# Optimization experiments

Hardware: AMD Instinct MI355X
Metric: run time of the kernel (lower is better)

## Reference

```python
import jax, jax.numpy as jnp
import numpy as np

SLOPE = 0.01

def leaky_tanh(x):
    return jnp.tanh(x * (2.0 / 3.0)) * 1.7159 + x * SLOPE

def lstm_cell(x, h, c, w_ih, w_hh, b_ih, b_hh):
    # torch LSTMCell gate order: i, f, g, o
    gates = x @ w_ih.T + b_ih + h @ w_hh.T + b_hh
    i, f, g, o = jnp.split(gates, 4, axis=-1)
    c_new = jax.nn.sigmoid(f) * c + jax.nn.sigmoid(i) * jnp.tanh(g)
    h_new = jax.nn.sigmoid(o) * jnp.tanh(c_new)
    return h_new, c_new

def setup_inputs() -> dict:
    key = jax.random.key(0)
    ks = jax.random.split(key, 16)
    T, B, I, H, O = 512, 64, 128, 2048, 64
    H1, H2 = H // 2, H // 8  # 1024, 256
    F2 = H // 4              # 512
    s = 0.02
    return {
        "inputs": jax.random.normal(ks[0], (T, B, I), dtype=jnp.float32),
        "fc1_w": jax.random.normal(ks[1], (H, I), dtype=jnp.float32) * s,
        "fc1_b": jax.random.normal(ks[2], (H,), dtype=jnp.float32) * s,
        "w_ih1": jax.random.normal(ks[3], (4 * H1, H), dtype=jnp.float32) * s,
        "w_hh1": jax.random.normal(ks[4], (4 * H1, H1), dtype=jnp.float32) * s,
        "b_ih1": jax.random.normal(ks[5], (4 * H1,), dtype=jnp.float32) * s,
        "b_hh1": jax.random.normal(ks[6], (4 * H1,), dtype=jnp.float32) * s,
        "fc2_w": jax.random.normal(ks[7], (F2, H1), dtype=jnp.float32) * s,
        "fc2_b": jax.random.normal(ks[8], (F2,), dtype=jnp.float32) * s,
        "w_ih2": jax.random.normal(ks[9], (4 * H2, F2), dtype=jnp.float32) * s,
        "w_hh2": jax.random.normal(ks[10], (4 * H2, H2), dtype=jnp.float32) * s,
        "b_ih2": jax.random.normal(ks[11], (4 * H2,), dtype=jnp.float32) * s,
        "b_hh2": jax.random.normal(ks[12], (4 * H2,), dtype=jnp.float32) * s,
        "fc3_w": jax.random.normal(ks[13], (O, H2), dtype=jnp.float32) * s,
        "fc3_b": jax.random.normal(ks[14], (O,), dtype=jnp.float32) * s,
    }

def reference(inputs, fc1_w, fc1_b, w_ih1, w_hh1, b_ih1, b_hh1,
              fc2_w, fc2_b, w_ih2, w_hh2, b_ih2, b_hh2, fc3_w, fc3_b):
    T, B, _ = inputs.shape
    H1 = w_hh1.shape[1]
    H2 = w_hh2.shape[1]
    h1 = jnp.zeros((B, H1), dtype=inputs.dtype)
    c1 = jnp.zeros((B, H1), dtype=inputs.dtype)
    h2 = jnp.zeros((B, H2), dtype=inputs.dtype)
    c2 = jnp.zeros((B, H2), dtype=inputs.dtype)

    def step(carry, xt):
        h1, c1, h2, c2 = carry
        x = leaky_tanh(xt @ fc1_w.T + fc1_b)
        h1, c1 = lstm_cell(x, h1, c1, w_ih1, w_hh1, b_ih1, b_hh1)
        x = leaky_tanh(h1 @ fc2_w.T + fc2_b)
        h2, c2 = lstm_cell(x, h2, c2, w_ih2, w_hh2, b_ih2, b_hh2)
        yhat = h2 @ fc3_w.T + fc3_b
        return (h1, c1, h2, c2), yhat

    _, outputs = jax.lax.scan(step, (h1, c1, h2, c2), inputs)
    return outputs  # [T, B, output_size]
```

## Files before the change

kernel.cpp:

```cpp
#include <hip/hip_runtime.h>
#include <hip/hip_bf16.h>

static constexpr int T_  = 512;
static constexpr int B_  = 64;
static constexpr int I_  = 128;
static constexpr int H_  = 2048;
static constexpr int H1_ = 1024;
static constexpr int F2_ = 512;
static constexpr int H2_ = 256;
static constexpr int O_  = 64;
static constexpr int G1N = 4096;
static constexpr int G2N = 1024;
static constexpr int NW  = 176;

typedef __attribute__((ext_vector_type(8))) __bf16 bfx8;
typedef __attribute__((ext_vector_type(4))) __bf16 bfx4;
typedef __attribute__((ext_vector_type(4))) float  fx4;

#define DEV __device__ __forceinline__

DEV fx4 mfma16(bfx8 a, bfx8 b, fx4 c) {
  return __builtin_amdgcn_mfma_f32_16x16x32_bf16(a, b, c, 0, 0, 0);
}
DEV float fast_sig(float x) { return 1.0f / (1.0f + __expf(-x)); }
DEV float fast_tanh(float x) {
  x = fminf(fmaxf(x, -30.0f), 30.0f);
  return 2.0f / (1.0f + __expf(-2.0f * x)) - 1.0f;
}
DEV float leaky_tanh_(float x) { return fast_tanh(x * (2.0f / 3.0f)) * 1.7159f + 0.01f * x; }

DEV void gld16(const void* g, void* l) {
  __builtin_amdgcn_global_load_lds(
      (const __attribute__((address_space(1))) unsigned int*)g,
      (__attribute__((address_space(3))) unsigned int*)l, 16, 0, 0);
}
DEV void gld16c(const void* g, void* l) {
  __builtin_amdgcn_global_load_lds(
      (const __attribute__((address_space(1))) unsigned int*)g,
      (__attribute__((address_space(3))) unsigned int*)l, 16, 0, 17);
}
DEV void spin_ge(int* p, int tgt) {
  while (__hip_atomic_load(p, __ATOMIC_RELAXED, __HIP_MEMORY_SCOPE_AGENT) < tgt)
    __builtin_amdgcn_s_sleep(1);
}
DEV void stc2(unsigned short* p, unsigned short v) {
  __hip_atomic_store(p, v, __ATOMIC_RELAXED, __HIP_MEMORY_SCOPE_AGENT);
}
DEV unsigned long long ldc8(const void* p) {
  return __hip_atomic_load((const unsigned long long*)p, __ATOMIC_RELAXED,
                           __HIP_MEMORY_SCOPE_AGENT);
}
DEV unsigned short bf16bits(float f) {
  __bf16 h = (__bf16)f;
  return __builtin_bit_cast(unsigned short, h);
}
DEV void arrive1(int* p) {
  __hip_atomic_fetch_add(p, 1, __ATOMIC_RELAXED, __HIP_MEMORY_SCOPE_AGENT);
}

__global__ void k_f2b(const float* __restrict__ s, __bf16* __restrict__ d, int n4) {
  int i = blockIdx.x * blockDim.x + threadIdx.x;
  int st = gridDim.x * blockDim.x;
  for (; i < n4; i += st) {
    float4 v = ((const float4*)s)[i];
    bfx4 o = { (__bf16)v.x, (__bf16)v.y, (__bf16)v.z, (__bf16)v.w };
    ((bfx4*)d)[i] = o;
  }
}
__global__ void k_add2(const float* __restrict__ a, const float* __restrict__ b,
                       float* __restrict__ d, int n) {
  int i = blockIdx.x * blockDim.x + threadIdx.x;
  if (i < n) d[i] = a[i] + b[i];
}

__global__ void k_wre1(const float* __restrict__ w, __bf16* __restrict__ W2) {
  int v = blockIdx.x * 256 + threadIdx.x;
  int l = v & 63, kk = (v >> 6) & 31, g = (v >> 11) & 3, ng = v >> 13;
  int row = g * 1024 + ng * 16 + (l & 15);
  int k0  = kk * 32 + (l >> 4) * 8;
  const float* sp = w + (size_t)row * 1024 + k0;
  float4 v0 = ((const float4*)sp)[0];
  float4 v1 = ((const float4*)sp)[1];
  bfx8 o = { (__bf16)v0.x, (__bf16)v0.y, (__bf16)v0.z, (__bf16)v0.w,
             (__bf16)v1.x, (__bf16)v1.y, (__bf16)v1.z, (__bf16)v1.w };
  *(bfx8*)(W2 + (size_t)v * 8) = o;
}

DEV void gemm_tile(char* sm, const __bf16* __restrict__ A, const __bf16* __restrict__ W,
                   __bf16* __restrict__ outB, const float* __restrict__ bias,
                   int m0, int n0, int N, int K, int epi, int wt)
{
  char* As = sm;
  char* Ws = sm + 16384;
  const int tid = threadIdx.x, lane = tid & 63, wave = tid >> 6;
  const int wm = wave >> 1, wn = wave & 1;
  const int rr = lane & 15, hi = lane >> 4;
  fx4 acc[4][4] = {};
  for (int k0 = 0; k0 < K; k0 += 64) {
    __syncthreads();
#pragma unroll
    for (int i = 0; i < 4; ++i) {
      int idx = i * 256 + tid;
      int r = idx >> 3, cs = (idx & 7) ^ (r & 7);
      gld16(A + (size_t)(m0 + r) * K + k0 + cs * 8, As + idx * 16);
      gld16(W + (size_t)(n0 + r) * K + k0 + cs * 8, Ws + idx * 16);
    }
    __syncthreads();
#pragma unroll
    for (int kh = 0; kh < 2; ++kh) {
      bfx8 a[4], b[4];
      const int cg = kh * 4 + hi;
#pragma unroll
      for (int mi = 0; mi < 4; ++mi) {
        int ra = wm * 64 + mi * 16 + rr;
        a[mi] = *(const bfx8*)(As + ra * 128 + ((cg ^ (ra & 7)) << 4));
      }
#pragma unroll
      for (int ni = 0; ni < 4; ++ni) {
        int rb = wn * 64 + ni * 16 + rr;
        b[ni] = *(const bfx8*)(Ws + rb * 128 + ((cg ^ (rb & 7)) << 4));
      }
#pragma unroll
      for (int mi = 0; mi < 4; ++mi)
#pragma unroll
        for (int ni = 0; ni < 4; ++ni)
          acc[mi][ni] = mfma16(a[mi], b[ni], acc[mi][ni]);
    }
  }
  const int cr = hi * 4, cc = rr;
#pragma unroll
  for (int mi = 0; mi < 4; ++mi)
#pragma unroll
    for (int ni = 0; ni < 4; ++ni) {
      int col = n0 + wn * 64 + ni * 16 + cc;
#pragma unroll
      for (int r = 0; r < 4; ++r) {
        int row = m0 + wm * 64 + mi * 16 + cr + r;
        float v = acc[mi][ni][r] + bias[col];
        if (epi == 1) v = leaky_tanh_(v);
        if (wt) stc2((unsigned short*)outB + ((size_t)row * N + col), bf16bits(v));
        else    outB[(size_t)row * N + col] = (__bf16)v;
      }
    }
}

__launch_bounds__(256)
__global__ void k_gemm(const __bf16* __restrict__ A, const __bf16* __restrict__ W,
                       __bf16* __restrict__ outB, const float* __restrict__ bias,
                       int M, int N, int K, int epi)
{
  __shared__ __align__(16) char sm[32768];
  (void)M;
  gemm_tile(sm, A, W, outB, bias, blockIdx.y * 128, blockIdx.x * 128, N, K, epi, 0);
}

DEV void stage(char* dst, int rsB, const __bf16* __restrict__ src, size_t sStride,
               int n, int lg) {
  for (int idx = threadIdx.x; idx < n; idx += 256) {
    int r = idx >> lg, c = idx & ((1 << lg) - 1);
    *(bfx8*)(dst + r * rsB + ((c * 16) ^ ((r & 7) << 4))) =
        *(const bfx8*)(src + (size_t)r * sStride + c * 8);
  }
}

struct KP {
  const __bf16 *W2, *whh2b;
  const __bf16 *g1rd;  __bf16 *g1wr;
  const __bf16 *xcrd;  __bf16 *xcwr;
  const __bf16 *infc1;
  const __bf16 *h1rd;  const __bf16 *h1s0;  __bf16 *h1wr;
  __bf16 *x2c; __bf16 *g2;
  const __bf16 *wfc1, *wih1, *wfc2, *wih2;
  const float *bfc1, *bs1, *bfc2, *bs2;
  float *c1, *c2;
  __bf16 *h2a;
  int *cnt;
  int Tc, t2base, do_l1, do_l2, do_fc2, do_ih1, do_fc1;
};

__launch_bounds__(256, 1)
__global__ void k_persist3(KP p)
{
  __shared__ __align__(16) char smem[131072];
  const int tid = threadIdx.x, lane = tid & 63, wv = tid >> 6;
  const int rr = lane & 15, hi = lane >> 4;
  const int col = tid & 15, brow = tid >> 4;
  const int bid = blockIdx.x;
  int* cnt = p.cnt;
  const int Tc = p.Tc;

  if (bid < 64) {
    if (!p.do_l1) return;
    const int ng = bid;
    char* As = smem;
    float* Cp = (float*)smem;

    bfx8 wreg[4][8];
#pragma unroll
    for (int g = 0; g < 4; ++g)
#pragma unroll
      for (int j = 0; j < 8; ++j)
        wreg[g][j] = *(const bfx8*)(p.W2 + (size_t)((ng * 4 + g) * 32 + wv * 8 + j) * 512 + lane * 8);

    float pc[4];
#pragma unroll
    for (int q = 0; q < 4; ++q)
      pc[q] = p.c1[(brow + q * 16) * 1024 + ng * 16 + col];

    for (int s = 0; s < Tc; ++s) {
      float pg[4][4];
#pragma unroll
      for (int q = 0; q < 4; ++q)
#pragma unroll
        for (int g = 0; g < 4; ++g)
          pg[q][g] = (float)p.g1rd[(size_t)(s * 64 + brow + q * 16) * 4096 + g * 1024 + ng * 16 + col];

      if (s > 0 && tid < 4) spin_ge(cnt + tid * 128, 16 * s);
      __syncthreads();

      const __bf16* h1s = (s == 0) ? p.h1s0 : (p.h1wr + (size_t)s * 65536);
      {
        char* dstb = smem + wv * 32768;
#pragma unroll 8
        for (int i = 0; i < 32; ++i) {
          int d = wv * 2048 + i * 64 + lane;
          int r = d >> 7;
          int sg = (r << 7) | ((d & 127) ^ (r & 7));
          gld16c(h1s + (size_t)sg * 8, dstb + i * 1024);
        }
      }
      __syncthreads();

      fx4 acc[4][4] = {};
#pragma unroll
      for (int j = 0; j < 8; ++j) {
        const int kB = (wv * 8 + j) * 64 + hi * 16;
        bfx8 a[4];
#pragma unroll
        for (int m = 0; m < 4; ++m) {
          int ra = m * 16 + rr;
          a[m] = *(const bfx8*)(As + ra * 2048 + (kB ^ ((ra & 7) << 4)));
        }
#pragma unroll
        for (int g = 0; g < 4; ++g)
#pragma unroll
          for (int m = 0; m < 4; ++m)
            acc[g][m] = mfma16(a[m], wreg[g][j], acc[g][m]);
      }
      __syncthreads();
#pragma unroll
      for (int g = 0; g < 4; ++g)
#pragma unroll
        for (int m = 0; m < 4; ++m) {
          int gc = g * 16 + rr;
          int bx = (m * 16 + hi * 4) ^ ((gc & 15) << 2);
          *(fx4*)(Cp + ((wv * 64 + gc) * 64 + bx)) = acc[g][m];
        }
      __syncthreads();

      __bf16* h1o = p.h1wr + (size_t)(s + 1) * 65536;
#pragma unroll
      for (int q = 0; q < 4; ++q) {
        int b_ = brow + q * 16;
        float gv[4];
#pragma unroll
        for (int g = 0; g < 4; ++g) {
          int gc = g * 16 + col;
          int bx = b_ ^ ((gc & 15) << 2);
          float v = pg[q][g];
#pragma unroll
          for (int w = 0; w < 4; ++w)
            v += Cp[(w * 64 + gc) * 64 + bx];
          gv[g] = v;
        }
        float cn = fast_sig(gv[1]) * pc[q] + fast_sig(gv[0]) * fast_tanh(gv[2]);
        pc[q] = cn;
        float hv = fast_sig(gv[3]) * fast_tanh(cn);
        stc2((unsigned short*)h1o + (b_ * 1024 + ng * 16 + col), bf16bits(hv));
      }
      __syncthreads();
      if (tid == 0) arrive1(cnt + (ng & 3) * 128);
    }
#pragma unroll
    for (int q = 0; q < 4; ++q)
      p.c1[(brow + q * 16) * 1024 + ng * 16 + col] = pc[q];

  } else if (bid < 80) {
    if (!p.do_l2) return;
    const int ng2 = bid - 64;
    char* Ws2 = smem;
    char* As2 = smem + 32768;
    float (*Gx2)[64][16] = (float (*)[64][16])(smem + 32768);

    for (int idx = tid; idx < 2048; idx += 256) {
      int r = idx >> 5, c = idx & 31;
      int wr = (r >> 4) * 256 + ng2 * 16 + (r & 15);
      *(bfx8*)(Ws2 + r * 512 + ((c * 16) ^ ((r & 7) << 4))) =
          *(const bfx8*)(p.whh2b + (size_t)wr * 256 + c * 8);
    }
    float pc2[4];
#pragma unroll
    for (int q = 0; q < 4; ++q)
      pc2[q] = p.c2[(brow + q * 16) * 256 + ng2 * 16 + col];

    if (tid == 0) spin_ge(cnt + 640, NW);
    __syncthreads();

    for (int s = 0; s < Tc; ++s) {
      float pg[4][4];
#pragma unroll
      for (int q = 0; q < 4; ++q)
#pragma unroll
        for (int g = 0; g < 4; ++g)
          pg[q][g] = (float)p.g2[(size_t)(s * 64 + brow + q * 16) * 1024 + g * 256 + ng2 * 16 + col];

      if (s > 0 && tid == 0) spin_ge(cnt + 512, 16 * s);
      __syncthreads();

      const __bf16* h2s = p.h2a + (size_t)(p.t2base + s) * 16384;
      for (int idx = tid; idx < 2048; idx += 256) {
        int r = idx >> 5, c = idx & 31;
        const char* sp = (const char*)(h2s + r * 256 + c * 8);
        unsigned long long lo = ldc8(sp), hi8 = ldc8(sp + 8);
        char* dp = As2 + r * 512 + ((c * 16) ^ ((r & 7) << 4));
        *(unsigned long long*)dp = lo;
        *(unsigned long long*)(dp + 8) = hi8;
      }
      __syncthreads();

      fx4 acc[4] = {};
#pragma unroll
      for (int ks = 0; ks < 8; ++ks) {
        const int cb = ks * 64 + hi * 16;
        int rb = wv * 16 + rr;
        bfx8 bfr = *(const bfx8*)(Ws2 + rb * 512 + (cb ^ ((rb & 7) << 4)));
#pragma unroll
        for (int m = 0; m < 4; ++m) {
          int ra = m * 16 + rr;
          bfx8 afr = *(const bfx8*)(As2 + ra * 512 + (cb ^ ((ra & 7) << 4)));
          acc[m] = mfma16(afr, bfr, acc[m]);
        }
      }
      __syncthreads();
#pragma unroll
      for (int m = 0; m < 4; ++m)
#pragma unroll
        for (int r = 0; r < 4; ++r)
          Gx2[wv][m * 16 + hi * 4 + r][rr] = acc[m][r];
      __syncthreads();

      __bf16* h2o = p.h2a + (size_t)(p.t2base + s + 1) * 16384;
#pragma unroll
      for (int q = 0; q < 4; ++q) {
        int b_ = brow + q * 16;
        float gi = Gx2[0][b_][col] + pg[q][0];
        float gf = Gx2[1][b_][col] + pg[q][1];
        float gg = Gx2[2][b_][col] + pg[q][2];
        float go = Gx2[3][b_][col] + pg[q][3];
        float cn = fast_sig(gf) * pc2[q] + fast_sig(gi) * fast_tanh(gg);
        pc2[q] = cn;
        float hv = fast_sig(go) * fast_tanh(cn);
        stc2((unsigned short*)h2o + (b_ * 256 + ng2 * 16 + col), bf16bits(hv));
      }
      __syncthreads();
      if (tid == 0) arrive1(cnt + 512);
    }
#pragma unroll
    for (int q = 0; q < 4; ++q)
      p.c2[(brow + q * 16) * 256 + ng2 * 16 + col] = pc2[q];

  } else {
    const int wid = bid - 80;
    const int Mt = (Tc * 64) / 128;
    if (p.do_fc2) {
      for (int i = wid; i < Mt * 4; i += NW)
        gemm_tile(smem, p.h1rd + 65536, p.wfc2, p.x2c, p.bfc2,
                  (i >> 2) * 128, (i & 3) * 128, F2_, H1_, 1, 1);
      __syncthreads();
      if (tid == 0) { arrive1(cnt + 576); spin_ge(cnt + 576, NW); }
      __syncthreads();
      for (int i = wid; i < Mt * 8; i += NW)
        gemm_tile(smem, p.x2c, p.wih2, p.g2, p.bs2,
                  (i >> 3) * 128, (i & 7) * 128, G2N, F2_, 0, 1);
      __syncthreads();
      if (tid == 0) arrive1(cnt + 640);
    }
    if (p.do_ih1) {
      for (int i = wid; i < Mt * 32; i += NW)
        gemm_tile(smem, p.xcrd, p.wih1, p.g1wr, p.bs1,
                  (i >> 5) * 128, (i & 31) * 128, G1N, H_, 0, 0);
    }
    if (p.do_fc1) {
      for (int i = wid; i < Mt * 16; i += NW)
        gemm_tile(smem, p.infc1, p.wfc1, p.xcwr, p.bfc1,
                  (i >> 4) * 128, (i & 15) * 128, H_, I_, 1, 0);
    }
  }
}

__launch_bounds__(256)
__global__ void k_fc3b(const __bf16* __restrict__ H2mat, const __bf16* __restrict__ w3,
                       const float* __restrict__ b3, float* __restrict__ out)
{
  __shared__ __align__(16) char smem[65536];
  const int tid = threadIdx.x, lane = tid & 63, wv = tid >> 6;
  const int rr = lane & 15, hi = lane >> 4;
  char* As = smem;
  char* Ws = smem + 32768;
  const size_t row0 = (size_t)blockIdx.x * 64;
  stage(As, 512, H2mat + row0 * 256, 256, 2048, 5);
  stage(Ws, 512, w3, 256, 2048, 5);
  __syncthreads();
  fx4 acc[4] = {};
#pragma unroll
  for (int ks = 0; ks < 8; ++ks) {
    const int cbB = ks * 64 + hi * 16;
    int rb = wv * 16 + rr;
    bfx8 bfr = *(const bfx8*)(Ws + rb * 512 + (cbB ^ ((rb & 7) << 4)));
#pragma unroll
    for (int m = 0; m < 4; ++m) {
      int ra = m * 16 + rr;
      bfx8 afr = *(const bfx8*)(As + ra * 512 + (cbB ^ ((ra & 7) << 4)));
      acc[m] = mfma16(afr, bfr, acc[m]);
    }
  }
  float bv = b3[wv * 16 + rr];
#pragma unroll
  for (int m = 0; m < 4; ++m)
#pragma unroll
    for (int r = 0; r < 4; ++r)
      out[(row0 + m * 16 + hi * 4 + r) * 64 + wv * 16 + rr] = acc[m][r] + bv;
}

extern "C" void kernel_launch(void* const* d_in, const int* in_sizes, int n_in,
                              void* d_out, int out_size, void* d_ws, size_t ws_size,
                              hipStream_t stream)
{
  (void)in_sizes; (void)n_in; (void)out_size;
  const float* f_in = (const float*)d_in[0];
  const float* fc1w = (const float*)d_in[1];
  const float* fc1b = (const float*)d_in[2];
  const float* wih1 = (const float*)d_in[3];
  const float* whh1 = (const float*)d_in[4];
  const float* bih1 = (const float*)d_in[5];
  const float* bhh1 = (const float*)d_in[6];
  const float* fc2w = (const float*)d_in[7];
  const float* fc2b = (const float*)d_in[8];
  const float* wih2 = (const float*)d_in[9];
  const float* whh2 = (const float*)d_in[10];
  const float* bih2 = (const float*)d_in[11];
  const float* bhh2 = (const float*)d_in[12];
  const float* fc3w = (const float*)d_in[13];
  const float* fc3b = (const float*)d_in[14];
  float* out = (float*)d_out;

  char* base = (char*)d_ws;
  size_t off = 0;
  auto alloc = [&](size_t bytes) -> char* {
    char* q = base + off;
    off = (off + bytes + 255) & ~(size_t)255;
    return q;
  };
  __bf16* wb_fc1 = (__bf16*)alloc((size_t)H_ * I_ * 2);
  __bf16* wb_ih1 = (__bf16*)alloc((size_t)G1N * H_ * 2);
  __bf16* W2     = (__bf16*)alloc((size_t)G1N * H1_ * 2);
  __bf16* wb_fc2 = (__bf16*)alloc((size_t)F2_ * H1_ * 2);
  __bf16* wb_ih2 = (__bf16*)alloc((size_t)G2N * F2_ * 2);
  __bf16* wb_hh2 = (__bf16*)alloc((size_t)G2N * H2_ * 2);
  __bf16* wb_fc3 = (__bf16*)alloc((size_t)O_ * H2_ * 2);
  __bf16* in_bf  = (__bf16*)alloc((size_t)T_ * B_ * I_ * 2);
  float*  bsum1  = (float*) alloc((size_t)G1N * 4);
  float*  bsum2  = (float*) alloc((size_t)G2N * 4);
  float*  c1     = (float*) alloc((size_t)B_ * H1_ * 4);
  float*  c2     = (float*) alloc((size_t)B_ * H2_ * 4);
  __bf16* h2a    = (__bf16*)alloc((size_t)(T_ + 1) * B_ * H2_ * 2);
  __bf16* h1zero = (__bf16*)alloc((size_t)B_ * H1_ * 2);
  int*    cnt    = (int*)   alloc(4096);
  size_t fixed = off;

  auto perTc = [](size_t Tc) -> size_t {
    size_t Mc = Tc * 64;
    return 2 * Mc * H_ * 2
         + 2 * Mc * G1N * 2
         + 2 * (Tc + 1) * (size_t)B_ * H1_ * 2
         + Mc * F2_ * 2
         + Mc * G2N * 2
         + 10 * 256;
  };
  int Tc = 128;
  while (Tc > 2 && fixed + perTc(Tc) > ws_size) Tc >>= 1;
  const int Mc = Tc * 64;
  __bf16* XcA  = (__bf16*)alloc((size_t)Mc * H_ * 2);
  __bf16* XcB  = (__bf16*)alloc((size_t)Mc * H_ * 2);
  __bf16* G1A  = (__bf16*)alloc((size_t)Mc * G1N * 2);
  __bf16* G1B  = (__bf16*)alloc((size_t)Mc * G1N * 2);
  __bf16* h1rA = (__bf16*)alloc((size_t)(Tc + 1) * B_ * H1_ * 2);
  __bf16* h1rB = (__bf16*)alloc((size_t)(Tc + 1) * B_ * H1_ * 2);
  __bf16* x2c  = (__bf16*)alloc((size_t)Mc * F2_ * 2);
  __bf16* G2cb = (__bf16*)alloc((size_t)Mc * G2N * 2);

  struct CV { const float* s; __bf16* d; int n; } cvs[7] = {
    {fc1w, wb_fc1, H_ * I_},   {wih1, wb_ih1, G1N * H_},
    {fc2w, wb_fc2, F2_ * H1_}, {wih2, wb_ih2, G2N * F2_}, {whh2, wb_hh2, G2N * H2_},
    {fc3w, wb_fc3, O_ * H2_},  {f_in, in_bf, T_ * B_ * I_},
  };
  for (int i = 0; i < 7; ++i) {
    int n4 = cvs[i].n / 4;
    int blocks = (n4 + 255) / 256;
    if (blocks > 2048) blocks = 2048;
    k_f2b<<<blocks, 256, 0, stream>>>(cvs[i].s, cvs[i].d, n4);
  }
  k_wre1<<<2048, 256, 0, stream>>>(whh1, W2);
  k_add2<<<G1N / 256, 256, 0, stream>>>(bih1, bhh1, bsum1, G1N);
  k_add2<<<G2N / 256, 256, 0, stream>>>(bih2, bhh2, bsum2, G2N);
  hipMemsetAsync(c1, 0, (size_t)B_ * H1_ * 4, stream);
  hipMemsetAsync(c2, 0, (size_t)B_ * H2_ * 4, stream);
  hipMemsetAsync(h1zero, 0, (size_t)B_ * H1_ * 2, stream);
  hipMemsetAsync(h2a, 0, (size_t)B_ * H2_ * 2, stream);

  const int chunks = T_ / Tc;
  k_gemm<<<dim3(H_ / 128, Mc / 128), 256, 0, stream>>>(in_bf, wb_fc1, XcA, fc1b, Mc, H_, I_, 1);
  k_gemm<<<dim3(G1N / 128, Mc / 128), 256, 0, stream>>>(XcA, wb_ih1, G1A, bsum1, Mc, G1N, H_, 0);
  if (chunks > 1)
    k_gemm<<<dim3(H_ / 128, Mc / 128), 256, 0, stream>>>(
        in_bf + (size_t)Mc * I_, wb_fc1, XcB, fc1b, Mc, H_, I_, 1);

  KP p;
  p.W2 = W2; p.whh2b = wb_hh2;
  p.wfc1 = wb_fc1; p.wih1 = wb_ih1; p.wfc2 = wb_fc2; p.wih2 = wb_ih2;
  p.bfc1 = fc1b; p.bs1 = bsum1; p.bfc2 = fc2b; p.bs2 = bsum2;
  p.c1 = c1; p.c2 = c2; p.h2a = h2a; p.cnt = cnt;
  p.x2c = x2c; p.g2 = G2cb; p.Tc = Tc;

  for (int k = 0; k < chunks; ++k) {
    hipMemsetAsync(cnt, 0, 4096, stream);
    p.g1rd = (k & 1) ? G1B : G1A;
    p.g1wr = (k & 1) ? G1A : G1B;
    p.xcrd = ((k + 1) & 1) ? XcB : XcA;
    p.xcwr = (k & 1) ? XcB : XcA;
    p.infc1 = (k + 2 < chunks) ? (in_bf + (size_t)(k + 2) * Mc * I_) : in_bf;
    p.h1wr = (k & 1) ? h1rB : h1rA;
    p.h1rd = (k & 1) ? h1rA : h1rB;
    p.h1s0 = (k == 0) ? h1zero : (p.h1rd + (size_t)Tc * 65536);
    p.t2base = (k - 1) * Tc;
    p.do_l1 = 1;
    p.do_l2 = (k >= 1);
    p.do_fc2 = (k >= 1);
    p.do_ih1 = (k + 1 < chunks);
    p.do_fc1 = (k + 2 < chunks);
    k_persist3<<<256, 256, 0, stream>>>(p);
  }
  hipMemsetAsync(cnt, 0, 4096, stream);
  p.h1rd = ((chunks - 1) & 1) ? h1rB : h1rA;
  p.h1wr = p.h1rd == h1rA ? h1rB : h1rA;
  p.h1s0 = h1zero;
  p.g1rd = G1A; p.g1wr = G1B; p.xcrd = XcA; p.xcwr = XcB; p.infc1 = in_bf;
  p.t2base = (chunks - 1) * Tc;
  p.do_l1 = 0; p.do_l2 = 1; p.do_fc2 = 1; p.do_ih1 = 0; p.do_fc1 = 0;
  k_persist3<<<256, 256, 0, stream>>>(p);
  k_fc3b<<<(T_ * B_) / 64, 256, 0, stream>>>(h2a + (size_t)B_ * H2_, wb_fc3, fc3b, out);
}
```

Baseline: 3.350 ms.

## Load LSTM1 h-state straight into registers, vectorize cell epilogue, double-buffer GEMM

In the persistent layer-1 recurrence, each wave now reads its h1 A-fragments from global memory directly into registers. This replaces staging them into LDS with global_load_lds, and drops two block barriers from the per-step critical path. The gate epilogue is remapped so each thread handles four consecutive hidden units. This lets it use vector loads for the precomputed gates and cell state, and a single 8-byte atomic store for h. Separately, the batched GEMM gets a two-stage LDS double buffer so loads for the next k tile overlap compute on the current one. Risks: plain global loads replace the cache-policy loads previously used for cross-block h1 data, which may read stale data across XCDs, and register pressure grows from the 32 A-fragments held per wave.

```diff
diff --git a/kernel.cpp b/kernel.cpp
--- a/kernel.cpp
+++ b/kernel.cpp
@@ -34,16 +34,14 @@
       (const __attribute__((address_space(1))) unsigned int*)g,
       (__attribute__((address_space(3))) unsigned int*)l, 16, 0, 0);
 }
-DEV void gld16c(const void* g, void* l) {
-  __builtin_amdgcn_global_load_lds(
-      (const __attribute__((address_space(1))) unsigned int*)g,
-      (__attribute__((address_space(3))) unsigned int*)l, 16, 0, 17);
-}
 DEV void spin_ge(int* p, int tgt) {
   while (__hip_atomic_load(p, __ATOMIC_RELAXED, __HIP_MEMORY_SCOPE_AGENT) < tgt)
     __builtin_amdgcn_s_sleep(1);
 }
 DEV void stc2(unsigned short* p, unsigned short v) {
+  __hip_atomic_store(p, v, __ATOMIC_RELAXED, __HIP_MEMORY_SCOPE_AGENT);
+}
+DEV void stc8(unsigned long long* p, unsigned long long v) {
   __hip_atomic_store(p, v, __ATOMIC_RELAXED, __HIP_MEMORY_SCOPE_AGENT);
 }
 DEV unsigned long long ldc8(const void* p) {
@@ -90,14 +88,13 @@
                    __bf16* __restrict__ outB, const float* __restrict__ bias,
                    int m0, int n0, int N, int K, int epi, int wt)
 {
-  char* As = sm;
-  char* Ws = sm + 16384;
   const int tid = threadIdx.x, lane = tid & 63, wave = tid >> 6;
   const int wm = wave >> 1, wn = wave & 1;
   const int rr = lane & 15, hi = lane >> 4;
   fx4 acc[4][4] = {};
-  for (int k0 = 0; k0 < K; k0 += 64) {
-    __syncthreads();
+  auto issue = [&](int buf, int k0) {
+    char* As = sm + buf * 32768;
+    char* Ws = As + 16384;
 #pragma unroll
     for (int i = 0; i < 4; ++i) {
       int idx = i * 256 + tid;
@@ -105,7 +102,16 @@
       gld16(A + (size_t)(m0 + r) * K + k0 + cs * 8, As + idx * 16);
       gld16(W + (size_t)(n0 + r) * K + k0 + cs * 8, Ws + idx * 16);
     }
+  };
+  __syncthreads();
+  issue(0, 0);
+  int cur = 0;
+  for (int k0 = 0; k0 < K; k0 += 64) {
+    asm volatile("s_waitcnt vmcnt(0)" ::: "memory");
     __syncthreads();
+    if (k0 + 64 < K) issue(cur ^ 1, k0 + 64);
+    char* As = sm + cur * 32768;
+    char* Ws = As + 16384;
 #pragma unroll
     for (int kh = 0; kh < 2; ++kh) {
       bfx8 a[4], b[4];
@@ -126,6 +132,7 @@
         for (int ni = 0; ni < 4; ++ni)
           acc[mi][ni] = mfma16(a[mi], b[ni], acc[mi][ni]);
     }
+    cur ^= 1;
   }
   const int cr = hi * 4, cc = rr;
 #pragma unroll
@@ -149,7 +156,7 @@
                        __bf16* __restrict__ outB, const float* __restrict__ bias,
                        int M, int N, int K, int epi)
 {
-  __shared__ __align__(16) char sm[32768];
+  __shared__ __align__(16) char sm[65536];
   (void)M;
   gemm_tile(sm, A, W, outB, bias, blockIdx.y * 128, blockIdx.x * 128, N, K, epi, 0);
 }
@@ -184,7 +191,6 @@
   __shared__ __align__(16) char smem[131072];
   const int tid = threadIdx.x, lane = tid & 63, wv = tid >> 6;
   const int rr = lane & 15, hi = lane >> 4;
-  const int col = tid & 15, brow = tid >> 4;
   const int bid = blockIdx.x;
   int* cnt = p.cnt;
   const int Tc = p.Tc;
@@ -192,8 +198,9 @@
   if (bid < 64) {
     if (!p.do_l1) return;
     const int ng = bid;
-    char* As = smem;
     float* Cp = (float*)smem;
+    const int eb = tid >> 2;
+    const int ec = (tid & 3) * 4;
 
     bfx8 wreg[4][8];
 #pragma unroll
@@ -202,92 +209,79 @@
       for (int j = 0; j < 8; ++j)
         wreg[g][j] = *(const bfx8*)(p.W2 + (size_t)((ng * 4 + g) * 32 + wv * 8 + j) * 512 + lane * 8);
 
-    float pc[4];
-#pragma unroll
-    for (int q = 0; q < 4; ++q)
-      pc[q] = p.c1[(brow + q * 16) * 1024 + ng * 16 + col];
+    fx4 pcv = *(const fx4*)(p.c1 + eb * 1024 + ng * 16 + ec);
 
     for (int s = 0; s < Tc; ++s) {
-      float pg[4][4];
-#pragma unroll
-      for (int q = 0; q < 4; ++q)
+      bfx4 pgv[4];
+#pragma unroll
+      for (int g = 0; g < 4; ++g)
+        pgv[g] = *(const bfx4*)(p.g1rd + (size_t)(s * 64 + eb) * 4096 + g * 1024 + ng * 16 + ec);
+
+      if (s > 0 && tid < 4) spin_ge(cnt + tid * 128, 16 * s);
+      __syncthreads();
+      asm volatile("" ::: "memory");
+
+      const __bf16* h1s = (s == 0) ? p.h1s0 : (p.h1wr + (size_t)s * 65536);
+      bfx8 afr[8][4];
+#pragma unroll
+      for (int j = 0; j < 8; ++j)
+#pragma unroll
+        for (int m = 0; m < 4; ++m)
+          afr[j][m] = *(const bfx8*)(h1s + (size_t)(m * 16 + rr) * 1024 + (wv * 8 + j) * 32 + hi * 8);
+
+      fx4 acc[4][4] = {};
+#pragma unroll
+      for (int j = 0; j < 8; ++j)
 #pragma unroll
         for (int g = 0; g < 4; ++g)
-          pg[q][g] = (float)p.g1rd[(size_t)(s * 64 + brow + q * 16) * 4096 + g * 1024 + ng * 16 + col];
-
-      if (s > 0 && tid < 4) spin_ge(cnt + tid * 128, 16 * s);
-      __syncthreads();
-
-      const __bf16* h1s = (s == 0) ? p.h1s0 : (p.h1wr + (size_t)s * 65536);
-      {
-        char* dstb = smem + wv * 32768;
-#pragma unroll 8
-        for (int i = 0; i < 32; ++i) {
-          int d = wv * 2048 + i * 64 + lane;
-          int r = d >> 7;
-          int sg = (r << 7) | ((d & 127) ^ (r & 7));
-          gld16c(h1s + (size_t)sg * 8, dstb + i * 1024);
-        }
-      }
-      __syncthreads();
-
-      fx4 acc[4][4] = {};
-#pragma unroll
-      for (int j = 0; j < 8; ++j) {
-        const int kB = (wv * 8 + j) * 64 + hi * 16;
-        bfx8 a[4];
-#pragma unroll
-        for (int m = 0; m < 4; ++m) {
-          int ra = m * 16 + rr;
-          a[m] = *(const bfx8*)(As + ra * 2048 + (kB ^ ((ra & 7) << 4)));
-        }
-#pragma unroll
-        for (int g = 0; g < 4; ++g)
 #pragma unroll
           for (int m = 0; m < 4; ++m)
-            acc[g][m] = mfma16(a[m], wreg[g][j], acc[g][m]);
-      }
-      __syncthreads();
+            acc[g][m] = mfma16(afr[j][m], wreg[g][j], acc[g][m]);
+
 #pragma unroll
       for (int g = 0; g < 4; ++g)
 #pragma unroll
         for (int m = 0; m < 4; ++m) {
           int gc = g * 16 + rr;
-          int bx = (m * 16 + hi * 4) ^ ((gc & 15) << 2);
+          int bx = (m * 16 + hi * 4) ^ (rr << 2);
           *(fx4*)(Cp + ((wv * 64 + gc) * 64 + bx)) = acc[g][m];
         }
       __syncthreads();
 
       __bf16* h1o = p.h1wr + (size_t)(s + 1) * 65536;
-#pragma unroll
-      for (int q = 0; q < 4; ++q) {
-        int b_ = brow + q * 16;
+      float hv[4];
+#pragma unroll
+      for (int e = 0; e < 4; ++e) {
+        int c = ec + e;
+        int bx = eb ^ (c << 2);
         float gv[4];
 #pragma unroll
         for (int g = 0; g < 4; ++g) {
-          int gc = g * 16 + col;
-          int bx = b_ ^ ((gc & 15) << 2);
-          float v = pg[q][g];
+          int gc = g * 16 + c;
+          float v = (float)pgv[g][e];
 #pragma unroll
           for (int w = 0; w < 4; ++w)
             v += Cp[(w * 64 + gc) * 64 + bx];
           gv[g] = v;
         }
-        float cn = fast_sig(gv[1]) * pc[q] + fast_sig(gv[0]) * fast_tanh(gv[2]);
-        pc[q] = cn;
-        float hv = fast_sig(gv[3]) * fast_tanh(cn);
-        stc2((unsigned short*)h1o + (b_ * 1024 + ng * 16 + col), bf16bits(hv));
-      }
+        float cn = fast_sig(gv[1]) * pcv[e] + fast_sig(gv[0]) * fast_tanh(gv[2]);
+        pcv[e] = cn;
+        hv[e] = fast_sig(gv[3]) * fast_tanh(cn);
+      }
+      unsigned long long v8 =  (unsigned long long)bf16bits(hv[0])
+        | ((unsigned long long)bf16bits(hv[1]) << 16)
+        | ((unsigned long long)bf16bits(hv[2]) << 32)
+        | ((unsigned long long)bf16bits(hv[3]) << 48);
+      stc8((unsigned long long*)(h1o + eb * 1024 + ng * 16 + ec), v8);
       __syncthreads();
       if (tid == 0) arrive1(cnt + (ng & 3) * 128);
     }
-#pragma unroll
-    for (int q = 0; q < 4; ++q)
-      p.c1[(brow + q * 16) * 1024 + ng * 16 + col] = pc[q];
+    *(fx4*)(p.c1 + eb * 1024 + ng * 16 + ec) = pcv;
 
   } else if (bid < 80) {
     if (!p.do_l2) return;
     const int ng2 = bid - 64;
+    const int col = tid & 15, brow = tid >> 4;
     char* Ws2 = smem;
     char* As2 = smem + 32768;
     float (*Gx2)[64][16] = (float (*)[64][16])(smem + 32768);
```

After: 3.814 ms. +13.9%, slower.

## Fuse prep kernels, drop per-chunk counter resets, fold fc3 into persistent kernel

Applied to the files above, without the earlier changes.

Replaces the separate conversion, bias-add, reorder and memset launches with one prep kernel. Synchronisation counters now keep counting across chunk launches, so the per-chunk memsets go away. The fc1 GEMMs for the first two chunks are merged into one launch. The final fc3 projection moves into the last persistent kernel's worker blocks, which spin on layer-2 progress, and the separate fc3 kernel is removed. This cuts launch count and host/stream overhead, at the cost of more complex monotonic counter targets and a larger counter buffer.

```diff
diff --git a/kernel.cpp b/kernel.cpp
--- a/kernel.cpp
+++ b/kernel.cpp
@@ -58,32 +58,51 @@
   __hip_atomic_fetch_add(p, 1, __ATOMIC_RELAXED, __HIP_MEMORY_SCOPE_AGENT);
 }
 
-__global__ void k_f2b(const float* __restrict__ s, __bf16* __restrict__ d, int n4) {
-  int i = blockIdx.x * blockDim.x + threadIdx.x;
-  int st = gridDim.x * blockDim.x;
-  for (; i < n4; i += st) {
-    float4 v = ((const float4*)s)[i];
-    bfx4 o = { (__bf16)v.x, (__bf16)v.y, (__bf16)v.z, (__bf16)v.w };
-    ((bfx4*)d)[i] = o;
+struct PP {
+  const float *fc1w, *wih1f, *whh1f, *fc2w, *wih2f, *whh2f, *fc3w, *fin;
+  const float *bih1, *bhh1, *bih2, *bhh2;
+  __bf16 *wb_fc1, *wb_ih1, *W2, *wb_fc2, *wb_ih2, *wb_hh2, *wb_fc3, *in_bf;
+  float *bsum1, *bsum2, *c1, *c2;
+  __bf16 *h1zero, *h2a;
+  int *cnt;
+};
+__global__ void k_prep(PP q) {
+  const int bid = blockIdx.x, tid = threadIdx.x;
+  if (bid < 2048) {
+    int v = bid * 256 + tid;
+    int l = v & 63, kk = (v >> 6) & 31, g = (v >> 11) & 3, ng = v >> 13;
+    int row = g * 1024 + ng * 16 + (l & 15);
+    int k0  = kk * 32 + (l >> 4) * 8;
+    const float* sp = q.whh1f + (size_t)row * 1024 + k0;
+    float4 v0 = ((const float4*)sp)[0];
+    float4 v1 = ((const float4*)sp)[1];
+    bfx8 o = { (__bf16)v0.x, (__bf16)v0.y, (__bf16)v0.z, (__bf16)v0.w,
+               (__bf16)v1.x, (__bf16)v1.y, (__bf16)v1.z, (__bf16)v1.w };
+    *(bfx8*)(q.W2 + (size_t)v * 8) = o;
+    return;
   }
-}
-__global__ void k_add2(const float* __restrict__ a, const float* __restrict__ b,
-                       float* __restrict__ d, int n) {
-  int i = blockIdx.x * blockDim.x + threadIdx.x;
-  if (i < n) d[i] = a[i] + b[i];
-}
-
-__global__ void k_wre1(const float* __restrict__ w, __bf16* __restrict__ W2) {
-  int v = blockIdx.x * 256 + threadIdx.x;
-  int l = v & 63, kk = (v >> 6) & 31, g = (v >> 11) & 3, ng = v >> 13;
-  int row = g * 1024 + ng * 16 + (l & 15);
-  int k0  = kk * 32 + (l >> 4) * 8;
-  const float* sp = w + (size_t)row * 1024 + k0;
-  float4 v0 = ((const float4*)sp)[0];
-  float4 v1 = ((const float4*)sp)[1];
-  bfx8 o = { (__bf16)v0.x, (__bf16)v0.y, (__bf16)v0.z, (__bf16)v0.w,
-             (__bf16)v1.x, (__bf16)v1.y, (__bf16)v1.z, (__bf16)v1.w };
-  *(bfx8*)(W2 + (size_t)v * 8) = o;
+  const int gw = (bid - 2048) * 256 + tid, gs = 512 * 256;
+  for (int i = gw; i < 65536; i += gs) q.c1[i] = 0.0f;
+  for (int i = gw; i < 16384; i += gs) q.c2[i] = 0.0f;
+  for (int i = gw; i < 16384; i += gs) ((unsigned*)q.h1zero)[i] = 0u;
+  for (int i = gw; i < 8192;  i += gs) ((unsigned*)q.h2a)[i] = 0u;
+  for (int i = gw; i < 4096;  i += gs) q.cnt[i] = 0;
+  for (int i = gw; i < 4096; i += gs) q.bsum1[i] = q.bih1[i] + q.bhh1[i];
+  for (int i = gw; i < 1024; i += gs) q.bsum2[i] = q.bih2[i] + q.bhh2[i];
+  auto cv = [&](const float* s, __bf16* d, int n4) {
+    for (int i = gw; i < n4; i += gs) {
+      float4 v = ((const float4*)s)[i];
+      bfx4 o = { (__bf16)v.x, (__bf16)v.y, (__bf16)v.z, (__bf16)v.w };
+      ((bfx4*)d)[i] = o;
+    }
+  };
+  cv(q.fc1w,  q.wb_fc1, (H_ * I_) / 4);
+  cv(q.wih1f, q.wb_ih1, (G1N * H_) / 4);
+  cv(q.fc2w,  q.wb_fc2, (F2_ * H1_) / 4);
+  cv(q.wih2f, q.wb_ih2, (G2N * F2_) / 4);
+  cv(q.whh2f, q.wb_hh2, (G2N * H2_) / 4);
+  cv(q.fc3w,  q.wb_fc3, (O_ * H2_) / 4);
+  cv(q.fin,   q.in_bf,  (T_ * B_ * I_) / 4);
 }
 
 DEV void gemm_tile(char* sm, const __bf16* __restrict__ A, const __bf16* __restrict__ W,
@@ -163,19 +182,52 @@
   }
 }
 
+DEV void fc3_tile(char* smem, const __bf16* __restrict__ h2s,
+                  const __bf16* __restrict__ w3, const float* __restrict__ b3,
+                  float* __restrict__ out)
+{
+  const int tid = threadIdx.x, lane = tid & 63, wv = tid >> 6;
+  const int rr = lane & 15, hi = lane >> 4;
+  char* As = smem;
+  char* Ws = smem + 32768;
+  stage(As, 512, h2s, 256, 2048, 5);
+  stage(Ws, 512, w3, 256, 2048, 5);
+  __syncthreads();
+  fx4 acc[4] = {};
+#pragma unroll
+  for (int ks = 0; ks < 8; ++ks) {
+    const int cbB = ks * 64 + hi * 16;
+    int rb = wv * 16 + rr;
+    bfx8 bfr = *(const bfx8*)(Ws + rb * 512 + (cbB ^ ((rb & 7) << 4)));
+#pragma unroll
+    for (int m = 0; m < 4; ++m) {
+      int ra = m * 16 + rr;
+      bfx8 afr = *(const bfx8*)(As + ra * 512 + (cbB ^ ((ra & 7) << 4)));
+      acc[m] = mfma16(afr, bfr, acc[m]);
+    }
+  }
+  float bv = b3[wv * 16 + rr];
+#pragma unroll
+  for (int m = 0; m < 4; ++m)
+#pragma unroll
+    for (int r = 0; r < 4; ++r)
+      out[(m * 16 + hi * 4 + r) * 64 + wv * 16 + rr] = acc[m][r] + bv;
+}
+
 struct KP {
-  const __bf16 *W2, *whh2b;
+  const __bf16 *W2, *whh2b, *wfc3;
   const __bf16 *g1rd;  __bf16 *g1wr;
   const __bf16 *xcrd;  __bf16 *xcwr;
   const __bf16 *infc1;
   const __bf16 *h1rd;  const __bf16 *h1s0;  __bf16 *h1wr;
   __bf16 *x2c; __bf16 *g2;
   const __bf16 *wfc1, *wih1, *wfc2, *wih2;
-  const float *bfc1, *bs1, *bfc2, *bs2;
-  float *c1, *c2;
+  const float *bfc1, *bs1, *bfc2, *bs2, *b3;
+  float *c1, *c2, *out;
   __bf16 *h2a;
   int *cnt;
-  int Tc, t2base, do_l1, do_l2, do_fc2, do_ih1, do_fc1;
+  int Tc, t0, j0, fc2_tgt, ih2_tgt, pool_off;
+  int do_l1, do_l2, do_fc2, do_ih1, do_fc1, do_fc3;
 };
 
 __launch_bounds__(256, 1)
@@ -184,7 +236,6 @@
   __shared__ __align__(16) char smem[131072];
   const int tid = threadIdx.x, lane = tid & 63, wv = tid >> 6;
   const int rr = lane & 15, hi = lane >> 4;
-  const int col = tid & 15, brow = tid >> 4;
   const int bid = blockIdx.x;
   int* cnt = p.cnt;
   const int Tc = p.Tc;
@@ -194,6 +245,7 @@
     const int ng = bid;
     char* As = smem;
     float* Cp = (float*)smem;
+    const int col = tid & 15, brow = tid >> 4;
 
     bfx8 wreg[4][8];
 #pragma unroll
@@ -215,7 +267,7 @@
         for (int g = 0; g < 4; ++g)
           pg[q][g] = (float)p.g1rd[(size_t)(s * 64 + brow + q * 16) * 4096 + g * 1024 + ng * 16 + col];
 
-      if (s > 0 && tid < 4) spin_ge(cnt + tid * 128, 16 * s);
+      if (tid < 4) spin_ge(cnt + tid * 128, 16 * (p.t0 + s));
       __syncthreads();
 
       const __bf16* h1s = (s == 0) ? p.h1s0 : (p.h1wr + (size_t)s * 65536);
@@ -288,6 +340,7 @@
   } else if (bid < 80) {
     if (!p.do_l2) return;
     const int ng2 = bid - 64;
+    const int col = tid & 15, brow = tid >> 4;
     char* Ws2 = smem;
     char* As2 = smem + 32768;
     float (*Gx2)[64][16] = (float (*)[64][16])(smem + 32768);
@@ -303,7 +356,7 @@
     for (int q = 0; q < 4; ++q)
       pc2[q] = p.c2[(brow + q * 16) * 256 + ng2 * 16 + col];
 
-    if (tid == 0) spin_ge(cnt + 640, NW);
+    if (tid == 0) spin_ge(cnt + 640, p.ih2_tgt);
     __syncthreads();
 
     for (int s = 0; s < Tc; ++s) {
@@ -314,10 +367,10 @@
         for (int g = 0; g < 4; ++g)
           pg[q][g] = (float)p.g2[(size_t)(s * 64 + brow + q * 16) * 1024 + g * 256 + ng2 * 16 + col];
 
-      if (s > 0 && tid == 0) spin_ge(cnt + 512, 16 * s);
-      __syncthreads();
-
-      const __bf16* h2s = p.h2a + (size_t)(p.t2base + s) * 16384;
+      if (tid == 0) spin_ge(cnt + 512, 16 * (p.j0 + s));
+      __syncthreads();
+
+      const __bf16* h2s = p.h2a + (size_t)(p.j0 + s) * 16384;
       for (int idx = tid; idx < 2048; idx += 256) {
         int r = idx >> 5, c = idx & 31;
         const char* sp = (const char*)(h2s + r * 256 + c * 8);
@@ -349,7 +402,7 @@
           Gx2[wv][m * 16 + hi * 4 + r][rr] = acc[m][r];
       __syncthreads();
 
-      __bf16* h2o = p.h2a + (size_t)(p.t2base + s + 1) * 16384;
+      __bf16* h2o = p.h2a + (size_t)(p.j0 + s + 1) * 16384;
 #pragma unroll
       for (int q = 0; q < 4; ++q) {
         int b_ = brow + q * 16;
@@ -377,7 +430,7 @@
         gemm_tile(smem, p.h1rd + 65536, p.wfc2, p.x2c, p.bfc2,
                   (i >> 2) * 128, (i & 3) * 128, F2_, H1_, 1, 1);
       __syncthreads();
-      if (tid == 0) { arrive1(cnt + 576); spin_ge(cnt + 576, NW); }
+      if (tid == 0) { arrive1(cnt + 576); spin_ge(cnt + 576, p.fc2_tgt); }
       __syncthreads();
       for (int i = wid; i < Mt * 8; i += NW)
         gemm_tile(smem, p.x2c, p.wih2, p.g2, p.bs2,
@@ -395,41 +448,16 @@
         gemm_tile(smem, p.infc1, p.wfc1, p.xcwr, p.bfc1,
                   (i >> 4) * 128, (i & 15) * 128, H_, I_, 1, 0);
     }
+    if (p.do_fc3) {
+      for (int t = wid; t < T_; t += NW) {
+        if (tid == 0) spin_ge(cnt + 512, 16 * (t + 1));
+        __syncthreads();
+        fc3_tile(smem, p.h2a + (size_t)(t + 1) * 16384, p.wfc3, p.b3,
+                 p.out + (size_t)t * 4096);
+        __syncthreads();
+      }
+    }
   }
-}
-
-__launch_bounds__(256)
-__global__ void k_fc3b(const __bf16* __restrict__ H2mat, const __bf16* __restrict__ w3,
-                       const float* __restrict__ b3, float* __restrict__ out)
-{
-  __shared__ __align__(16) char smem[65536];
-  const int tid = threadIdx.x, lane = tid & 63, wv = tid >> 6;
-  const int rr = lane & 15, hi = lane >> 4;
-  char* As = smem;
-  char* Ws = smem + 32768;
-  const size_t row0 = (size_t)blockIdx.x * 64;
-  stage(As, 512, H2mat + row0 * 256, 256, 2048, 5);
-  stage(Ws, 512, w3, 256, 2048, 5);
-  __syncthreads();
-  fx4 acc[4] = {};
-#pragma unroll
-  for (int ks = 0; ks < 8; ++ks) {
-    const int cbB = ks * 64 + hi * 16;
-    int rb = wv * 16 + rr;
-    bfx8 bfr = *(const bfx8*)(Ws + rb * 512 + (cbB ^ ((rb & 7) << 4)));
-#pragma unroll
-    for (int m = 0; m < 4; ++m) {
-      int ra = m * 16 + rr;
-      bfx8 afr = *(const bfx8*)(As + ra * 512 + (cbB ^ ((ra & 7) << 4)));
-      acc[m] = mfma16(afr, bfr, acc[m]);
-    }
-  }
-  float bv = b3[wv * 16 + rr];
-#pragma unroll
-  for (int m = 0; m < 4; ++m)
-#pragma unroll
-    for (int r = 0; r < 4; ++r)
-      out[(row0 + m * 16 + hi * 4 + r) * 64 + wv * 16 + rr] = acc[m][r] + bv;
 }
 
 extern "C" void kernel_launch(void* const* d_in, const int* in_sizes, int n_in,
@@ -475,20 +503,17 @@
   float*  c2     = (float*) alloc((size_t)B_ * H2_ * 4);
   __bf16* h2a    = (__bf16*)alloc((size_t)(T_ + 1) * B_ * H2_ * 2);
   __bf16* h1zero = (__bf16*)alloc((size_t)B_ * H1_ * 2);
-  int*    cnt    = (int*)   alloc(4096);
+  int*    cnt    = (int*)   alloc(16384);
   size_t fixed = off;
 
   auto perTc = [](size_t Tc) -> size_t {
     size_t Mc = Tc * 64;
-    return 2 * Mc * H_ * 2
-         + 2 * Mc * G1N * 2
+    return 2 * Mc * H_ * 2 + 2 * Mc * G1N * 2
          + 2 * (Tc + 1) * (size_t)B_ * H1_ * 2
-         + Mc * F2_ * 2
-         + Mc * G2N * 2
-         + 10 * 256;
+         + Mc * F2_ * 2 + Mc * G2N * 2 + 10 * 256;
   };
   int Tc = 128;
-  while (Tc > 2 && fixed + perTc(Tc) > ws_size) Tc >>= 1;
+  while (Tc > 8 && fixed + perTc(Tc) > ws_size) Tc >>= 1;
   const int Mc = Tc * 64;
   __bf16* XcA  = (__bf16*)alloc((size_t)Mc * H_ * 2);
   __bf16* XcB  = (__bf16*)alloc((size_t)Mc * H_ * 2);
@@ -499,41 +524,30 @@
   __bf16* x2c  = (__bf16*)alloc((size_t)Mc * F2_ * 2);
   __bf16* G2cb = (__bf16*)alloc((size_t)Mc * G2N * 2);
 
-  struct CV { const float* s; __bf16* d; int n; } cvs[7] = {
-    {fc1w, wb_fc1, H_ * I_},   {wih1, wb_ih1, G1N * H_},
-    {fc2w, wb_fc2, F2_ * H1_}, {wih2, wb_ih2, G2N * F2_}, {whh2, wb_hh2, G2N * H2_},
-    {fc3w, wb_fc3, O_ * H2_},  {f_in, in_bf, T_ * B_ * I_},
-  };
-  for (int i = 0; i < 7; ++i) {
-    int n4 = cvs[i].n / 4;
-    int blocks = (n4 + 255) / 256;
-    if (blocks > 2048) blocks = 2048;
-    k_f2b<<<blocks, 256, 0, stream>>>(cvs[i].s, cvs[i].d, n4);
-  }
-  k_wre1<<<2048, 256, 0, stream>>>(whh1, W2);
-  k_add2<<<G1N / 256, 256, 0, stream>>>(bih1, bhh1, bsum1, G1N);
-  k_add2<<<G2N / 256, 256, 0, stream>>>(bih2, bhh2, bsum2, G2N);
-  hipMemsetAsync(c1, 0, (size_t)B_ * H1_ * 4, stream);
-  hipMemsetAsync(c2, 0, (size_t)B_ * H2_ * 4, stream);
-  hipMemsetAsync(h1zero, 0, (size_t)B_ * H1_ * 2, stream);
-  hipMemsetAsync(h2a, 0, (size_t)B_ * H2_ * 2, stream);
+  PP q;
+  q.fc1w = fc1w; q.wih1f = wih1; q.whh1f = whh1; q.fc2w = fc2w;
+  q.wih2f = wih2; q.whh2f = whh2; q.fc3w = fc3w; q.fin = f_in;
+  q.bih1 = bih1; q.bhh1 = bhh1; q.bih2 = bih2; q.bhh2 = bhh2;
+  q.wb_fc1 = wb_fc1; q.wb_ih1 = wb_ih1; q.W2 = W2; q.wb_fc2 = wb_fc2;
+  q.wb_ih2 = wb_ih2; q.wb_hh2 = wb_hh2; q.wb_fc3 = wb_fc3; q.in_bf = in_bf;
+  q.bsum1 = bsum1; q.bsum2 = bsum2; q.c1 = c1; q.c2 = c2;
+  q.h1zero = h1zero; q.h2a = h2a; q.cnt = cnt;
+  k_prep<<<2560, 256, 0, stream>>>(q);
 
   const int chunks = T_ / Tc;
-  k_gemm<<<dim3(H_ / 128, Mc / 128), 256, 0, stream>>>(in_bf, wb_fc1, XcA, fc1b, Mc, H_, I_, 1);
-  k_gemm<<<dim3(G1N / 128, Mc / 128), 256, 0, stream>>>(XcA, wb_ih1, G1A, bsum1, Mc, G1N, H_, 0);
-  if (chunks > 1)
-    k_gemm<<<dim3(H_ / 128, Mc / 128), 256, 0, stream>>>(
-        in_bf + (size_t)Mc * I_, wb_fc1, XcB, fc1b, Mc, H_, I_, 1);
+  k_gemm<<<dim3(H_ / 128, (2 * Mc) / 128), 256, 0, stream>>>(
+      in_bf, wb_fc1, XcA, fc1b, 2 * Mc, H_, I_, 1);
+  k_gemm<<<dim3(G1N / 128, Mc / 128), 256, 0, stream>>>(
+      XcA, wb_ih1, G1A, bsum1, Mc, G1N, H_, 0);
 
   KP p;
-  p.W2 = W2; p.whh2b = wb_hh2;
+  p.W2 = W2; p.whh2b = wb_hh2; p.wfc3 = wb_fc3;
   p.wfc1 = wb_fc1; p.wih1 = wb_ih1; p.wfc2 = wb_fc2; p.wih2 = wb_ih2;
-  p.bfc1 = fc1b; p.bs1 = bsum1; p.bfc2 = fc2b; p.bs2 = bsum2;
-  p.c1 = c1; p.c2 = c2; p.h2a = h2a; p.cnt = cnt;
+  p.bfc1 = fc1b; p.bs1 = bsum1; p.bfc2 = fc2b; p.bs2 = bsum2; p.b3 = fc3b;
+  p.c1 = c1; p.c2 = c2; p.h2a = h2a; p.cnt = cnt; p.out = out;
   p.x2c = x2c; p.g2 = G2cb; p.Tc = Tc;
 
   for (int k = 0; k < chunks; ++k) {
-    hipMemsetAsync(cnt, 0, 4096, stream);
     p.g1rd = (k & 1) ? G1B : G1A;
     p.g1wr = (k & 1) ? G1A : G1B;
     p.xcrd = ((k + 1) & 1) ? XcB : XcA;
@@ -542,21 +556,28 @@
     p.h1wr = (k & 1) ? h1rB : h1rA;
     p.h1rd = (k & 1) ? h1rA : h1rB;
     p.h1s0 = (k == 0) ? h1zero : (p.h1rd + (size_t)Tc * 65536);
-    p.t2base = (k - 1) * Tc;
+    p.t0 = k * Tc;
+    p.j0 = (k - 1) * Tc;
+    p.fc2_tgt = NW * k;
+    p.ih2_tgt = NW * k;
+    p.pool_off = 2816 + k * 16;
     p.do_l1 = 1;
     p.do_l2 = (k >= 1);
     p.do_fc2 = (k >= 1);
     p.do_ih1 = (k + 1 < chunks);
     p.do_fc1 = (k + 2 < chunks);
+    p.do_fc3 = 0;
     k_persist3<<<256, 256, 0, stream>>>(p);
   }
-  hipMemsetAsync(cnt, 0, 4096, stream);
   p.h1rd = ((chunks - 1) & 1) ? h1rB : h1rA;
-  p.h1wr = p.h1rd == h1rA ? h1rB : h1rA;
+  p.h1wr = (p.h1rd == h1rA) ? h1rB : h1rA;
   p.h1s0 = h1zero;
   p.g1rd = G1A; p.g1wr = G1B; p.xcrd = XcA; p.xcwr = XcB; p.infc1 = in_bf;
-  p.t2base = (chunks - 1) * Tc;
-  p.do_l1 = 0; p.do_l2 = 1; p.do_fc2 = 1; p.do_ih1 = 0; p.do_fc1 = 0;
+  p.t0 = 0;
+  p.j0 = (chunks - 1) * Tc;
+  p.fc2_tgt = NW * chunks;
+  p.ih2_tgt = NW * chunks;
+  p.pool_off = 2816 + chunks * 16;
+  p.do_l1 = 0; p.do_l2 = 1; p.do_fc2 = 1; p.do_ih1 = 0; p.do_fc1 = 0; p.do_fc3 = 1;
   k_persist3<<<256, 256, 0, stream>>>(p);
-  k_fc3b<<<(T_ * B_) / 64, 256, 0, stream>>>(h2a + (size_t)B_ * H2_, wb_fc3, fc3b, out);
-}
+}
```

Result: no change. 3.376 ms (+0.8%).
